# Optimization experiments

Measured on AMD Instinct MI355X. Metric: run time of the kernel, lower is better.

Reference implementation:

```python
import jax, jax.numpy as jnp
import numpy as np

HEADS = 12
DIM_HEAD = 64

def setup_inputs() -> dict:
    key = jax.random.key(0)
    ks = jax.random.split(key, 5)
    B, S, D = 4, 2048, 768
    s = 0.02
    return {
        "x": jax.random.normal(ks[0], (B, S, D), dtype=jnp.float32),
        "Wq": jax.random.normal(ks[1], (D, D), dtype=jnp.float32) * s,
        "Wk": jax.random.normal(ks[2], (D, D), dtype=jnp.float32) * s,
        "Wv": jax.random.normal(ks[3], (D, D), dtype=jnp.float32) * s,
        "Wo": jax.random.normal(ks[4], (D, D), dtype=jnp.float32) * s,
        "bo": jnp.zeros((D,), dtype=jnp.float32),
    }

def reference(x, Wq, Wk, Wv, Wo, bo):
    B, S, D = x.shape
    H, Dh = HEADS, DIM_HEAD
    scale = Dh ** -0.5
    # projections (torch Linear: x @ W^T)
    q = (x @ Wq.T).reshape(B, S, H, Dh).transpose(0, 2, 1, 3) * scale  # [B,H,S,Dh]
    k = (x @ Wk.T).reshape(B, S, H, Dh).transpose(0, 2, 1, 3)
    v = (x @ Wv.T).reshape(B, S, H, Dh).transpose(0, 2, 1, 3)
    sim = jnp.einsum("bhid,bhjd->bhij", q, k)  # [B,H,S,S]
    mask_value = -jnp.finfo(sim.dtype).max
    causal_mask = jnp.triu(jnp.ones((S, S), dtype=bool), k=1)
    sim = jnp.where(causal_mask, mask_value, sim)
    attn = jax.nn.softmax(sim, axis=-1)
    # dropout is identity in eval mode
    out = jnp.einsum("bhij,bhjd->bhid", attn, v)  # [B,H,S,Dh]
    out = out.transpose(0, 2, 1, 3).reshape(B, S, H * Dh)
    return out @ Wo.T + bo
```

## Files before the change

kernel.cpp:

```cpp
#include <hip/hip_runtime.h>
#include <stdint.h>

typedef unsigned short u16;
typedef __bf16 bf16x8 __attribute__((ext_vector_type(8)));
typedef float f32x4 __attribute__((ext_vector_type(4)));
typedef u16 u16x4 __attribute__((ext_vector_type(4)));
typedef u16 u16x8 __attribute__((ext_vector_type(8)));
typedef uint32_t u32x2 __attribute__((ext_vector_type(2)));

#define LDS_CAST(p) (reinterpret_cast<__attribute__((address_space(3))) uint32_t*>(reinterpret_cast<uintptr_t>(p)))
#define GLB_CAST(p) (reinterpret_cast<const __attribute__((address_space(1))) uint32_t*>(reinterpret_cast<uintptr_t>(p)))
#define GLOAD16(g, l) __builtin_amdgcn_global_load_lds(GLB_CAST(g), LDS_CAST(l), 16, 0, 0)
#define AS3U16(p) (reinterpret_cast<__attribute__((address_space(3))) u16*>(reinterpret_cast<uintptr_t>(p)))

__device__ __forceinline__ u16 f2bf(float f) {
    uint32_t u = __builtin_bit_cast(uint32_t, f);
    u += 0x7fffu + ((u >> 16) & 1u);
    return (u16)(u >> 16);
}
__device__ __forceinline__ u16 bfbits(float f) {
    return __builtin_bit_cast(u16, (__bf16)f);
}

__global__ void cast_f32_bf16(const float* __restrict__ in, u16* __restrict__ out, int n4) {
    int i = blockIdx.x * blockDim.x + threadIdx.x;
    if (i >= n4) return;
    float4 f = reinterpret_cast<const float4*>(in)[i];
    u16x4 o;
    o.x = f2bf(f.x); o.y = f2bf(f.y); o.z = f2bf(f.z); o.w = f2bf(f.w);
    reinterpret_cast<u16x4*>(out)[i] = o;
}

__global__ void cast_w4(const float* __restrict__ a, const float* __restrict__ b,
                        const float* __restrict__ c, const float* __restrict__ d,
                        u16* __restrict__ oa, u16* __restrict__ ob,
                        u16* __restrict__ oc, u16* __restrict__ od, int n4) {
    const int z = blockIdx.y;
    const float* in = (z == 0) ? a : (z == 1) ? b : (z == 2) ? c : d;
    u16* out = (z == 0) ? oa : (z == 1) ? ob : (z == 2) ? oc : od;
    int i = blockIdx.x * blockDim.x + threadIdx.x;
    if (i >= n4) return;
    float4 f = reinterpret_cast<const float4*>(in)[i];
    u16x4 o;
    o.x = f2bf(f.x); o.y = f2bf(f.y); o.z = f2bf(f.z); o.w = f2bf(f.w);
    reinterpret_cast<u16x4*>(out)[i] = o;
}

__global__ __launch_bounds__(256) void gemm_qkv(
    const u16* __restrict__ X, const u16* __restrict__ Wq,
    const u16* __restrict__ Wk, const u16* __restrict__ Wv,
    u16* __restrict__ qo, u16* __restrict__ ko, u16* __restrict__ vTo)
{
    __shared__ u16 As[2][128 * 32];
    __shared__ u16 Bs[2][128 * 32];
    const int tid = threadIdx.x;
    const int lane = tid & 63;
    const int w = tid >> 6;
    const int lr = lane & 15, lg = lane >> 4;
    const int wrow = (w >> 1) * 64, wcol = (w & 1) * 64;

    const int lin = blockIdx.x + blockIdx.y * 6 + blockIdx.z * 384;
    const int xcd = lin & 7, idx = lin >> 3;
    const int prow = xcd * 8 + idx / 18;
    const int rem = idx % 18;
    const int bxc = rem % 6, z = rem / 6;
    const int row0 = prow * 128, col0 = bxc * 128;
    const u16* Wt = (z == 0) ? Wq : (z == 1) ? Wk : Wv;

    f32x4 acc[4][4];
#pragma unroll
    for (int m = 0; m < 4; ++m)
#pragma unroll
        for (int n = 0; n < 4; ++n)
#pragma unroll
            for (int j = 0; j < 4; ++j) acc[m][n][j] = 0.f;

#define QSTAGE(KT)                                                                                 \
    {                                                                                              \
        const int buf_ = (KT) & 1;                                                                 \
        _Pragma("unroll")                                                                          \
        for (int it = 0; it < 2; ++it) {                                                           \
            const int c = it * 256 + w * 64 + lane;                                                \
            const int row = c >> 2, c16 = c & 3;                                                   \
            GLOAD16(X  + (size_t)(row0 + row) * 768 + (KT) * 32 + c16 * 8, &As[buf_][(it * 256 + w * 64) * 8]); \
            GLOAD16(Wt + (size_t)(col0 + row) * 768 + (KT) * 32 + c16 * 8, &Bs[buf_][(it * 256 + w * 64) * 8]); \
        }                                                                                          \
    }

#define QSTEP(KT, VN, PF)                                                                          \
    {                                                                                              \
        if (PF) QSTAGE((KT) + 1);                                                                  \
        asm volatile("s_waitcnt vmcnt(" #VN ")" ::: "memory");                                     \
        __builtin_amdgcn_s_barrier();                                                              \
        const int cur_ = (KT) & 1;                                                                 \
        bf16x8 af[4], bfr[4];                                                                      \
        _Pragma("unroll")                                                                          \
        for (int m = 0; m < 4; ++m) af[m] = *(const bf16x8*)&As[cur_][(wrow + m * 16 + lr) * 32 + lg * 8]; \
        _Pragma("unroll")                                                                          \
        for (int n = 0; n < 4; ++n) bfr[n] = *(const bf16x8*)&Bs[cur_][(wcol + n * 16 + lr) * 32 + lg * 8]; \
        asm volatile("s_waitcnt lgkmcnt(0)" ::: "memory");                                         \
        __builtin_amdgcn_sched_barrier(0);                                                         \
        __builtin_amdgcn_s_barrier();                                                              \
        _Pragma("unroll")                                                                          \
        for (int m = 0; m < 4; ++m)                                                                \
            _Pragma("unroll")                                                                      \
            for (int n = 0; n < 4; ++n)                                                            \
                acc[m][n] = __builtin_amdgcn_mfma_f32_16x16x32_bf16(af[m], bfr[n], acc[m][n], 0, 0, 0); \
    }

    QSTAGE(0);
    for (int kt = 0; kt < 23; ++kt) QSTEP(kt, 4, true);
    QSTEP(23, 0, false);
#undef QSTEP
#undef QSTAGE

    if (z == 2) {
#pragma unroll
        for (int n = 0; n < 4; ++n) {
            const int j = col0 + wcol + n * 16 + lr;
            const int h = j >> 6, dh = j & 63;
#pragma unroll
            for (int m = 0; m < 4; ++m) {
                const int i0 = row0 + wrow + m * 16 + lg * 4;
                const int b = i0 >> 11, s0 = i0 & 2047;
                u16x4 pk;
#pragma unroll
                for (int r = 0; r < 4; ++r) pk[r] = bfbits(acc[m][n][r]);
                *(u16x4*)&vTo[(((size_t)b * 12 + h) * 64 + dh) * 2048 + s0] = pk;
            }
        }
    } else {
        u16* outp = (z == 0) ? qo : ko;
        const float scl = (z == 0) ? 0.18033688011112042f : 1.0f;
#pragma unroll
        for (int n = 0; n < 4; ++n) {
            const int j = col0 + wcol + n * 16 + lr;
            const int h = j >> 6, dh = j & 63;
#pragma unroll
            for (int m = 0; m < 4; ++m)
#pragma unroll
                for (int r = 0; r < 4; ++r) {
                    const int i = row0 + wrow + m * 16 + lg * 4 + r;
                    const int b = i >> 11, s = i & 2047;
                    outp[(((size_t)b * 12 + h) * 2048 + s) * 64 + dh] = bfbits(acc[m][n][r] * scl);
                }
        }
    }
}

template<bool DIAG>
__device__ __forceinline__ void attn_step(
    const bf16x8* aq, f32x4* o, float* lrow,
    const u16* __restrict__ Ksb, const u16* __restrict__ Vsb, u16* __restrict__ PT,
    int kvb, int qg0, int lr, int lg)
{
    f32x4 sacc[4];
#pragma unroll
    for (int n = 0; n < 4; ++n)
#pragma unroll
        for (int j = 0; j < 4; ++j) sacc[n][j] = 0.f;
    __builtin_amdgcn_s_setprio(1);
#pragma unroll
    for (int kk = 0; kk < 2; ++kk)
#pragma unroll
        for (int n = 0; n < 4; ++n) {
            const int row = n * 16 + lr;
            const int p = (kk * 4 + lg) ^ (row & 7);
            bf16x8 bk = *(const bf16x8*)&Ksb[row * 64 + p * 8];
            sacc[n] = __builtin_amdgcn_mfma_f32_16x16x32_bf16(aq[kk], bk, sacc[n], 0, 0, 0);
        }
    __builtin_amdgcn_s_setprio(0);

    float pv[4][4];
#pragma unroll
    for (int r = 0; r < 4; ++r) {
        float ls = 0.f;
#pragma unroll
        for (int n = 0; n < 4; ++n) {
            float sv = sacc[n][r];
            if (DIAG && (kvb + n * 16 + lr) > qg0 + r) sv = -1e30f;
            const float e = __builtin_amdgcn_exp2f(sv);
            pv[r][n] = e;
            ls += e;
        }
        lrow[r] += ls;
    }

#pragma unroll
    for (int n = 0; n < 4; ++n) {
        u16x4 pk;
#pragma unroll
        for (int r = 0; r < 4; ++r) pk[r] = bfbits(pv[r][n]);
        *(u16x4*)&PT[(n * 16 + lr) * 16 + lg * 4] = pk;
    }

    u32x2 t0, t1, t2, t3;
    __attribute__((address_space(3))) u16* pb = AS3U16(PT) + lg * 128 + lr * 4;
    asm volatile("ds_read_b64_tr_b16 %0, %1" : "=v"(t0) : "v"(pb) : "memory");
    asm volatile("ds_read_b64_tr_b16 %0, %1 offset:128" : "=v"(t1) : "v"(pb) : "memory");
    asm volatile("ds_read_b64_tr_b16 %0, %1 offset:1024" : "=v"(t2) : "v"(pb) : "memory");
    asm volatile("ds_read_b64_tr_b16 %0, %1 offset:1152" : "=v"(t3) : "v"(pb) : "memory");
    asm volatile("s_waitcnt lgkmcnt(0)" ::: "memory");
    __builtin_amdgcn_sched_barrier(0);
    union { u32x2 h[2]; bf16x8 v; } ua, ub;
    ua.h[0] = t0; ua.h[1] = t1;
    ub.h[0] = t2; ub.h[1] = t3;
    const bf16x8 ap0 = ua.v, ap1 = ub.v;

    __builtin_amdgcn_s_setprio(1);
#pragma unroll
    for (int n = 0; n < 4; ++n) {
        const int rowv = n * 16 + lr;
        const int p0 = (0 + lg) ^ (rowv & 7);
        const int p1 = (4 + lg) ^ (rowv & 7);
        bf16x8 bv0 = *(const bf16x8*)&Vsb[rowv * 64 + p0 * 8];
        bf16x8 bv1 = *(const bf16x8*)&Vsb[rowv * 64 + p1 * 8];
        o[n] = __builtin_amdgcn_mfma_f32_16x16x32_bf16(ap0, bv0, o[n], 0, 0, 0);
        o[n] = __builtin_amdgcn_mfma_f32_16x16x32_bf16(ap1, bv1, o[n], 0, 0, 0);
    }
    __builtin_amdgcn_s_setprio(0);
}

__global__ __launch_bounds__(256) void attn_kernel(
    const u16* __restrict__ q, const u16* __restrict__ k,
    const u16* __restrict__ vT, u16* __restrict__ attn)
{
    __shared__ u16 Ks[2][64 * 64];
    __shared__ u16 Vs[2][64 * 64];
    __shared__ u16 Ps[4][64 * 16];

    const int lin = blockIdx.x + (blockIdx.y << 4);
    const int logi = (lin & 7) * 96 + (lin >> 3);
    const int pair = logi & 15, bh = logi >> 4;

    const int qA = pair, qB = 31 - pair;
    const int tid = threadIdx.x, lane = tid & 63, w = tid >> 6;
    const int lr = lane & 15, lg = lane >> 4;

    const u16* Kp = k + (size_t)bh * 2048 * 64;
    const u16* Vp = vT + (size_t)bh * 64 * 2048;

    const u16* QpA = q + ((size_t)bh * 2048 + qA * 64 + w * 16) * 64;
    const u16* QpB = q + ((size_t)bh * 2048 + qB * 64 + w * 16) * 64;
    bf16x8 aqA[2], aqB[2];
    aqA[0] = *(const bf16x8*)&QpA[lr * 64 + lg * 8];
    aqA[1] = *(const bf16x8*)&QpA[lr * 64 + 32 + lg * 8];
    aqB[0] = *(const bf16x8*)&QpB[lr * 64 + lg * 8];
    aqB[1] = *(const bf16x8*)&QpB[lr * 64 + 32 + lg * 8];

    f32x4 oA[4], oB[4];
    float lA[4], lB[4];
#pragma unroll
    for (int n = 0; n < 4; ++n)
#pragma unroll
        for (int j = 0; j < 4; ++j) { oA[n][j] = 0.f; oB[n][j] = 0.f; }
#pragma unroll
    for (int r = 0; r < 4; ++r) { lA[r] = 0.f; lB[r] = 0.f; }

#define STAGE(T, BUF)                                                                        \
    {                                                                                        \
        _Pragma("unroll")                                                                    \
        for (int it = 0; it < 2; ++it) {                                                     \
            const int c = it * 256 + w * 64 + lane;                                          \
            const int row = c >> 3, pc = c & 7;                                              \
            const int lc = pc ^ (row & 7);                                                   \
            GLOAD16(Kp + (size_t)((T) * 64 + row) * 64 + lc * 8, &Ks[BUF][(it * 256 + w * 64) * 8]); \
            GLOAD16(Vp + (size_t)row * 2048 + (T) * 64 + lc * 8, &Vs[BUF][(it * 256 + w * 64) * 8]); \
        }                                                                                    \
    }

    STAGE(0, 0);
    const int qg0A = qA * 64 + w * 16 + lg * 4;
    const int qg0B = qB * 64 + w * 16 + lg * 4;

    int t = 0;
    for (; t < qA; ++t) {
        const int cur = t & 1;
        __syncthreads();
        STAGE(t + 1, cur ^ 1);
        attn_step<false>(aqB, oB, lB, Ks[cur], Vs[cur], Ps[w], t * 64, qg0B, lr, lg);
        attn_step<false>(aqA, oA, lA, Ks[cur], Vs[cur], Ps[w], t * 64, qg0A, lr, lg);
    }
    {
        const int cur = t & 1;
        __syncthreads();
        STAGE(t + 1, cur ^ 1);
        attn_step<false>(aqB, oB, lB, Ks[cur], Vs[cur], Ps[w], t * 64, qg0B, lr, lg);
        attn_step<true >(aqA, oA, lA, Ks[cur], Vs[cur], Ps[w], t * 64, qg0A, lr, lg);
        ++t;
    }
    for (; t < qB; ++t) {
        const int cur = t & 1;
        __syncthreads();
        STAGE(t + 1, cur ^ 1);
        attn_step<false>(aqB, oB, lB, Ks[cur], Vs[cur], Ps[w], t * 64, qg0B, lr, lg);
    }
    {
        const int cur = t & 1;
        __syncthreads();
        attn_step<true >(aqB, oB, lB, Ks[cur], Vs[cur], Ps[w], t * 64, qg0B, lr, lg);
    }
#undef STAGE

#pragma unroll
    for (int r = 0; r < 4; ++r) {
#pragma unroll
        for (int off = 1; off < 16; off <<= 1) {
            lA[r] += __shfl_xor(lA[r], off);
            lB[r] += __shfl_xor(lB[r], off);
        }
        lA[r] = 1.f / lA[r];
        lB[r] = 1.f / lB[r];
    }

    const int b = bh / 12, h = bh - b * 12;
#pragma unroll
    for (int n = 0; n < 4; ++n)
#pragma unroll
        for (int r = 0; r < 4; ++r) {
            const int sA = qA * 64 + w * 16 + lg * 4 + r;
            const int sB = qB * 64 + w * 16 + lg * 4 + r;
            attn[((size_t)b * 2048 + sA) * 768 + h * 64 + n * 16 + lr] = bfbits(oA[n][r] * lA[r]);
            attn[((size_t)b * 2048 + sB) * 768 + h * 64 + n * 16 + lr] = bfbits(oB[n][r] * lB[r]);
        }
}

__global__ __launch_bounds__(256) void gemm_out(
    const u16* __restrict__ A, const u16* __restrict__ Wo,
    const float* __restrict__ bo, float* __restrict__ out)
{
    __shared__ u16 As[2][128 * 32];
    __shared__ u16 Bs[2][128 * 32];
    const int tid = threadIdx.x;
    const int lane = tid & 63;
    const int w = tid >> 6;
    const int lr = lane & 15, lg = lane >> 4;
    const int wrow = (w >> 1) * 64, wcol = (w & 1) * 64;

    const int lin = blockIdx.x + blockIdx.y * 6;
    const int xcd = lin & 7, idx = lin >> 3;
    const int prow = xcd * 8 + idx / 6;
    const int bxc = idx % 6;
    const int row0 = prow * 128, col0 = bxc * 128;

    f32x4 acc[4][4];
#pragma unroll
    for (int m = 0; m < 4; ++m)
#pragma unroll
        for (int n = 0; n < 4; ++n)
#pragma unroll
            for (int j = 0; j < 4; ++j) acc[m][n][j] = 0.f;

#define OSTAGE(KT)                                                                                 \
    {                                                                                              \
        const int buf_ = (KT) & 1;                                                                 \
        _Pragma("unroll")                                                                          \
        for (int it = 0; it < 2; ++it) {                                                           \
            const int c = it * 256 + w * 64 + lane;                                                \
            const int row = c >> 2, c16 = c & 3;                                                   \
            GLOAD16(A  + (size_t)(row0 + row) * 768 + (KT) * 32 + c16 * 8, &As[buf_][(it * 256 + w * 64) * 8]); \
            GLOAD16(Wo + (size_t)(col0 + row) * 768 + (KT) * 32 + c16 * 8, &Bs[buf_][(it * 256 + w * 64) * 8]); \
        }                                                                                          \
    }

#define OSTEP(KT, VN, PF)                                                                          \
    {                                                                                              \
        if (PF) OSTAGE((KT) + 1);                                                                  \
        asm volatile("s_waitcnt vmcnt(" #VN ")" ::: "memory");                                     \
        __builtin_amdgcn_s_barrier();                                                              \
        const int cur_ = (KT) & 1;                                                                 \
        bf16x8 af[4], bfr[4];                                                                      \
        _Pragma("unroll")                                                                          \
        for (int m = 0; m < 4; ++m) af[m] = *(const bf16x8*)&As[cur_][(wrow + m * 16 + lr) * 32 + lg * 8]; \
        _Pragma("unroll")                                                                          \
        for (int n = 0; n < 4; ++n) bfr[n] = *(const bf16x8*)&Bs[cur_][(wcol + n * 16 + lr) * 32 + lg * 8]; \
        asm volatile("s_waitcnt lgkmcnt(0)" ::: "memory");                                         \
        __builtin_amdgcn_sched_barrier(0);                                                         \
        __builtin_amdgcn_s_barrier();                                                              \
        _Pragma("unroll")                                                                          \
        for (int m = 0; m < 4; ++m)                                                                \
            _Pragma("unroll")                                                                      \
            for (int n = 0; n < 4; ++n)                                                            \
                acc[m][n] = __builtin_amdgcn_mfma_f32_16x16x32_bf16(af[m], bfr[n], acc[m][n], 0, 0, 0); \
    }

    OSTAGE(0);
    for (int kt = 0; kt < 23; ++kt) OSTEP(kt, 4, true);
    OSTEP(23, 0, false);
#undef OSTEP
#undef OSTAGE

#pragma unroll
    for (int n = 0; n < 4; ++n) {
        const int j = col0 + wcol + n * 16 + lr;
        const float bj = bo[j];
#pragma unroll
        for (int m = 0; m < 4; ++m)
#pragma unroll
            for (int r = 0; r < 4; ++r) {
                const int i = row0 + wrow + m * 16 + lg * 4 + r;
                out[(size_t)i * 768 + j] = acc[m][n][r] + bj;
            }
    }
}

extern "C" void kernel_launch(void* const* d_in, const int* in_sizes, int n_in,
                              void* d_out, int out_size, void* d_ws, size_t ws_size,
                              hipStream_t stream) {
    const float* x  = (const float*)d_in[0];
    const float* Wq = (const float*)d_in[1];
    const float* Wk = (const float*)d_in[2];
    const float* Wv = (const float*)d_in[3];
    const float* Wo = (const float*)d_in[4];
    const float* bo = (const float*)d_in[5];
    float* out = (float*)d_out;

    const size_t NX = 6291456;
    const size_t NW = 589824;
    if (ws_size < (NX * 4 + NW * 4 + NX) * sizeof(u16)) return;
    u16* ws  = (u16*)d_ws;
    u16* xb  = ws;
    u16* wqb = xb  + NX;
    u16* wkb = wqb + NW;
    u16* wvb = wkb + NW;
    u16* wob = wvb + NW;
    u16* qb_ = wob + NW;
    u16* kb_ = qb_ + NX;
    u16* vtb = kb_ + NX;
    u16* ab_ = vtb + NX;

    cast_f32_bf16<<<6144, 256, 0, stream>>>(x, xb, (int)(NX / 4));
    cast_w4<<<dim3(576, 4), 256, 0, stream>>>(Wq, Wk, Wv, Wo, wqb, wkb, wvb, wob, (int)(NW / 4));

    gemm_qkv<<<dim3(6, 64, 3), 256, 0, stream>>>(xb, wqb, wkb, wvb, qb_, kb_, vtb);
    attn_kernel<<<dim3(16, 48), 256, 0, stream>>>(qb_, kb_, vtb, ab_);
    gemm_out<<<dim3(6, 64), 256, 0, stream>>>(ab_, wob, bo, out);
}
```

Baseline: 127.8 us.

## Compute transposed scores so P feeds PV MFMA from registers, skip LDS round-trip

The attention step now computes S^T by swapping MFMA operands, so each lane holds probabilities already laid out as the B operand of a 16x16x16 bf16 MFMA. That removes the per-wave LDS write and transposing reads of P, along with their wait. V tiles are now loaded through registers into a padded (stride 72) LDS layout instead of async global-to-LDS. Output stores are vectorized to 4 elements. In exchange, the PV product uses twice as many smaller-K MFMAs, and the V staging adds register pressure plus synchronous global loads.

```diff
diff --git a/kernel.cpp b/kernel.cpp
--- a/kernel.cpp
+++ b/kernel.cpp
@@ -6,12 +6,11 @@
 typedef float f32x4 __attribute__((ext_vector_type(4)));
 typedef u16 u16x4 __attribute__((ext_vector_type(4)));
 typedef u16 u16x8 __attribute__((ext_vector_type(8)));
-typedef uint32_t u32x2 __attribute__((ext_vector_type(2)));
+typedef short s16x4 __attribute__((ext_vector_type(4)));
 
 #define LDS_CAST(p) (reinterpret_cast<__attribute__((address_space(3))) uint32_t*>(reinterpret_cast<uintptr_t>(p)))
 #define GLB_CAST(p) (reinterpret_cast<const __attribute__((address_space(1))) uint32_t*>(reinterpret_cast<uintptr_t>(p)))
 #define GLOAD16(g, l) __builtin_amdgcn_global_load_lds(GLB_CAST(g), LDS_CAST(l), 16, 0, 0)
-#define AS3U16(p) (reinterpret_cast<__attribute__((address_space(3))) u16*>(reinterpret_cast<uintptr_t>(p)))
 
 __device__ __forceinline__ u16 f2bf(float f) {
     uint32_t u = __builtin_bit_cast(uint32_t, f);
@@ -150,9 +149,9 @@
 
 template<bool DIAG>
 __device__ __forceinline__ void attn_step(
-    const bf16x8* aq, f32x4* o, float* lrow,
-    const u16* __restrict__ Ksb, const u16* __restrict__ Vsb, u16* __restrict__ PT,
-    int kvb, int qg0, int lr, int lg)
+    const bf16x8* aq, f32x4* o, float& lsum,
+    const u16* __restrict__ Ksb, const u16* __restrict__ Vsb,
+    int kvb, int qgl, int lr, int lg)
 {
     f32x4 sacc[4];
 #pragma unroll
@@ -166,58 +165,39 @@
         for (int n = 0; n < 4; ++n) {
             const int row = n * 16 + lr;
             const int p = (kk * 4 + lg) ^ (row & 7);
-            bf16x8 bk = *(const bf16x8*)&Ksb[row * 64 + p * 8];
-            sacc[n] = __builtin_amdgcn_mfma_f32_16x16x32_bf16(aq[kk], bk, sacc[n], 0, 0, 0);
+            bf16x8 ak = *(const bf16x8*)&Ksb[row * 64 + p * 8];
+            sacc[n] = __builtin_amdgcn_mfma_f32_16x16x32_bf16(ak, aq[kk], sacc[n], 0, 0, 0);
         }
     __builtin_amdgcn_s_setprio(0);
 
-    float pv[4][4];
-#pragma unroll
-    for (int r = 0; r < 4; ++r) {
+    s16x4 pb[4];
+#pragma unroll
+    for (int n = 0; n < 4; ++n) {
         float ls = 0.f;
 #pragma unroll
-        for (int n = 0; n < 4; ++n) {
+        for (int r = 0; r < 4; ++r) {
             float sv = sacc[n][r];
-            if (DIAG && (kvb + n * 16 + lr) > qg0 + r) sv = -1e30f;
+            if (DIAG && (kvb + n * 16 + lg * 4 + r) > qgl) sv = -1e30f;
             const float e = __builtin_amdgcn_exp2f(sv);
-            pv[r][n] = e;
+            pb[n][r] = (short)bfbits(e);
             ls += e;
         }
-        lrow[r] += ls;
-    }
-
-#pragma unroll
-    for (int n = 0; n < 4; ++n) {
-        u16x4 pk;
-#pragma unroll
-        for (int r = 0; r < 4; ++r) pk[r] = bfbits(pv[r][n]);
-        *(u16x4*)&PT[(n * 16 + lr) * 16 + lg * 4] = pk;
-    }
-
-    u32x2 t0, t1, t2, t3;
-    __attribute__((address_space(3))) u16* pb = AS3U16(PT) + lg * 128 + lr * 4;
-    asm volatile("ds_read_b64_tr_b16 %0, %1" : "=v"(t0) : "v"(pb) : "memory");
-    asm volatile("ds_read_b64_tr_b16 %0, %1 offset:128" : "=v"(t1) : "v"(pb) : "memory");
-    asm volatile("ds_read_b64_tr_b16 %0, %1 offset:1024" : "=v"(t2) : "v"(pb) : "memory");
-    asm volatile("ds_read_b64_tr_b16 %0, %1 offset:1152" : "=v"(t3) : "v"(pb) : "memory");
-    asm volatile("s_waitcnt lgkmcnt(0)" ::: "memory");
-    __builtin_amdgcn_sched_barrier(0);
-    union { u32x2 h[2]; bf16x8 v; } ua, ub;
-    ua.h[0] = t0; ua.h[1] = t1;
-    ub.h[0] = t2; ub.h[1] = t3;
-    const bf16x8 ap0 = ua.v, ap1 = ub.v;
+        lsum += ls;
+    }
 
     __builtin_amdgcn_s_setprio(1);
 #pragma unroll
-    for (int n = 0; n < 4; ++n) {
-        const int rowv = n * 16 + lr;
-        const int p0 = (0 + lg) ^ (rowv & 7);
-        const int p1 = (4 + lg) ^ (rowv & 7);
-        bf16x8 bv0 = *(const bf16x8*)&Vsb[rowv * 64 + p0 * 8];
-        bf16x8 bv1 = *(const bf16x8*)&Vsb[rowv * 64 + p1 * 8];
-        o[n] = __builtin_amdgcn_mfma_f32_16x16x32_bf16(ap0, bv0, o[n], 0, 0, 0);
-        o[n] = __builtin_amdgcn_mfma_f32_16x16x32_bf16(ap1, bv1, o[n], 0, 0, 0);
-    }
+    for (int m = 0; m < 4; ++m)
+#pragma unroll
+        for (int n = 0; n < 4; ++n) {
+            s16x4 va = *(const s16x4*)&Vsb[(m * 16 + lr) * 72 + n * 16 + lg * 4];
+#if __has_builtin(__builtin_amdgcn_mfma_f32_16x16x16bf16_1k)
+            o[m] = __builtin_amdgcn_mfma_f32_16x16x16bf16_1k(va, pb[n], o[m], 0, 0, 0);
+#else
+            asm volatile("s_nop 3\n\tv_mfma_f32_16x16x16_bf16 %0, %1, %2, %0\n\ts_nop 4"
+                         : "+v"(o[m]) : "v"(va), "v"(pb[n]));
+#endif
+        }
     __builtin_amdgcn_s_setprio(0);
 }
 
@@ -225,9 +205,8 @@
     const u16* __restrict__ q, const u16* __restrict__ k,
     const u16* __restrict__ vT, u16* __restrict__ attn)
 {
-    __shared__ u16 Ks[2][64 * 64];
-    __shared__ u16 Vs[2][64 * 64];
-    __shared__ u16 Ps[4][64 * 16];
+    __shared__ __align__(16) u16 Ks[2][64 * 64];
+    __shared__ __align__(16) u16 Vs[2][64 * 72];
 
     const int lin = blockIdx.x + (blockIdx.y << 4);
     const int logi = (lin & 7) * 96 + (lin >> 3);
@@ -249,80 +228,89 @@
     aqB[1] = *(const bf16x8*)&QpB[lr * 64 + 32 + lg * 8];
 
     f32x4 oA[4], oB[4];
-    float lA[4], lB[4];
+    float lA = 0.f, lB = 0.f;
 #pragma unroll
     for (int n = 0; n < 4; ++n)
 #pragma unroll
         for (int j = 0; j < 4; ++j) { oA[n][j] = 0.f; oB[n][j] = 0.f; }
-#pragma unroll
-    for (int r = 0; r < 4; ++r) { lA[r] = 0.f; lB[r] = 0.f; }
-
-#define STAGE(T, BUF)                                                                        \
+
+    const int sc0 = w * 64 + lane;
+    const int srow0 = sc0 >> 3, spc0 = sc0 & 7;
+    const int srow1 = srow0 + 32;
+    const int lc0 = spc0 ^ (srow0 & 7);
+
+    float4 vr0, vr1;
+#define STAGE_V_LOAD(T)                                                                      \
     {                                                                                        \
-        _Pragma("unroll")                                                                    \
-        for (int it = 0; it < 2; ++it) {                                                     \
-            const int c = it * 256 + w * 64 + lane;                                          \
-            const int row = c >> 3, pc = c & 7;                                              \
-            const int lc = pc ^ (row & 7);                                                   \
-            GLOAD16(Kp + (size_t)((T) * 64 + row) * 64 + lc * 8, &Ks[BUF][(it * 256 + w * 64) * 8]); \
-            GLOAD16(Vp + (size_t)row * 2048 + (T) * 64 + lc * 8, &Vs[BUF][(it * 256 + w * 64) * 8]); \
-        }                                                                                    \
-    }
-
-    STAGE(0, 0);
-    const int qg0A = qA * 64 + w * 16 + lg * 4;
-    const int qg0B = qB * 64 + w * 16 + lg * 4;
+        vr0 = *(const float4*)(Vp + (size_t)srow0 * 2048 + (T) * 64 + spc0 * 8);             \
+        vr1 = *(const float4*)(Vp + (size_t)srow1 * 2048 + (T) * 64 + spc0 * 8);             \
+    }
+#define STAGE_K(T, BUF)                                                                      \
+    {                                                                                        \
+        GLOAD16(Kp + (size_t)((T) * 64 + srow0) * 64 + lc0 * 8, &Ks[BUF][sc0 * 8]);          \
+        GLOAD16(Kp + (size_t)((T) * 64 + srow1) * 64 + lc0 * 8, &Ks[BUF][(sc0 + 256) * 8]);  \
+    }
+#define STAGE_V_WRITE(BUF)                                                                   \
+    {                                                                                        \
+        *(float4*)&Vs[BUF][srow0 * 72 + spc0 * 8] = vr0;                                     \
+        *(float4*)&Vs[BUF][srow1 * 72 + spc0 * 8] = vr1;                                     \
+    }
+
+    STAGE_V_LOAD(0); STAGE_K(0, 0); STAGE_V_WRITE(0);
+
+    const int qglA = qA * 64 + w * 16 + lr;
+    const int qglB = qB * 64 + w * 16 + lr;
 
     int t = 0;
     for (; t < qA; ++t) {
         const int cur = t & 1;
         __syncthreads();
-        STAGE(t + 1, cur ^ 1);
-        attn_step<false>(aqB, oB, lB, Ks[cur], Vs[cur], Ps[w], t * 64, qg0B, lr, lg);
-        attn_step<false>(aqA, oA, lA, Ks[cur], Vs[cur], Ps[w], t * 64, qg0A, lr, lg);
+        STAGE_V_LOAD(t + 1); STAGE_K(t + 1, cur ^ 1);
+        attn_step<false>(aqB, oB, lB, Ks[cur], Vs[cur], t * 64, qglB, lr, lg);
+        STAGE_V_WRITE(cur ^ 1);
+        attn_step<false>(aqA, oA, lA, Ks[cur], Vs[cur], t * 64, qglA, lr, lg);
     }
     {
         const int cur = t & 1;
         __syncthreads();
-        STAGE(t + 1, cur ^ 1);
-        attn_step<false>(aqB, oB, lB, Ks[cur], Vs[cur], Ps[w], t * 64, qg0B, lr, lg);
-        attn_step<true >(aqA, oA, lA, Ks[cur], Vs[cur], Ps[w], t * 64, qg0A, lr, lg);
+        STAGE_V_LOAD(t + 1); STAGE_K(t + 1, cur ^ 1);
+        attn_step<false>(aqB, oB, lB, Ks[cur], Vs[cur], t * 64, qglB, lr, lg);
+        STAGE_V_WRITE(cur ^ 1);
+        attn_step<true >(aqA, oA, lA, Ks[cur], Vs[cur], t * 64, qglA, lr, lg);
         ++t;
     }
     for (; t < qB; ++t) {
         const int cur = t & 1;
         __syncthreads();
-        STAGE(t + 1, cur ^ 1);
-        attn_step<false>(aqB, oB, lB, Ks[cur], Vs[cur], Ps[w], t * 64, qg0B, lr, lg);
+        STAGE_V_LOAD(t + 1); STAGE_K(t + 1, cur ^ 1);
+        attn_step<false>(aqB, oB, lB, Ks[cur], Vs[cur], t * 64, qglB, lr, lg);
+        STAGE_V_WRITE(cur ^ 1);
     }
     {
         const int cur = t & 1;
         __syncthreads();
-        attn_step<true >(aqB, oB, lB, Ks[cur], Vs[cur], Ps[w], t * 64, qg0B, lr, lg);
-    }
-#undef STAGE
-
-#pragma unroll
-    for (int r = 0; r < 4; ++r) {
-#pragma unroll
-        for (int off = 1; off < 16; off <<= 1) {
-            lA[r] += __shfl_xor(lA[r], off);
-            lB[r] += __shfl_xor(lB[r], off);
-        }
-        lA[r] = 1.f / lA[r];
-        lB[r] = 1.f / lB[r];
-    }
+        attn_step<true >(aqB, oB, lB, Ks[cur], Vs[cur], t * 64, qglB, lr, lg);
+    }
+#undef STAGE_V_LOAD
+#undef STAGE_K
+#undef STAGE_V_WRITE
+
+    lA += __shfl_xor(lA, 16); lA += __shfl_xor(lA, 32);
+    lB += __shfl_xor(lB, 16); lB += __shfl_xor(lB, 32);
+    const float iA = 1.f / lA, iB = 1.f / lB;
 
     const int b = bh / 12, h = bh - b * 12;
-#pragma unroll
-    for (int n = 0; n < 4; ++n)
-#pragma unroll
-        for (int r = 0; r < 4; ++r) {
-            const int sA = qA * 64 + w * 16 + lg * 4 + r;
-            const int sB = qB * 64 + w * 16 + lg * 4 + r;
-            attn[((size_t)b * 2048 + sA) * 768 + h * 64 + n * 16 + lr] = bfbits(oA[n][r] * lA[r]);
-            attn[((size_t)b * 2048 + sB) * 768 + h * 64 + n * 16 + lr] = bfbits(oB[n][r] * lB[r]);
-        }
+    const int sA = qA * 64 + w * 16 + lr;
+    const int sB = qB * 64 + w * 16 + lr;
+#pragma unroll
+    for (int m = 0; m < 4; ++m) {
+        u16x4 pa, pbk;
+#pragma unroll
+        for (int r = 0; r < 4; ++r) { pa[r] = bfbits(oA[m][r] * iA); pbk[r] = bfbits(oB[m][r] * iB); }
+        const int dh0 = h * 64 + m * 16 + lg * 4;
+        *(u16x4*)&attn[((size_t)b * 2048 + sA) * 768 + dh0] = pa;
+        *(u16x4*)&attn[((size_t)b * 2048 + sB) * 768 + dh0] = pbk;
+    }
 }
 
 __global__ __launch_bounds__(256) void gemm_out(
```

After: 145.6 us. 13.9% more time.
